# Kernel optimization log

Hardware: AMD Instinct MI355X
Metric: run time of the kernel (lower is better)

## Reference

```python
import jax, jax.numpy as jnp
import numpy as np

N_FACTORS = 4
N_ITERATIONS = 2
N_LAYERS = 2
N_USERS = 50000
N_ITEMS = 50000
EMB_DIM = 128
N_EDGES = 2_000_000
EPS = 1e-12


def setup_inputs() -> dict:
    key = jax.random.key(0)
    k1, k2, k3, k4 = jax.random.split(key, 4)
    n_nodes = N_USERS + N_ITEMS
    return {
        "user_emb": jax.random.normal(k1, (N_USERS, EMB_DIM), dtype=jnp.float32) * 0.1,
        "item_emb": jax.random.normal(k2, (N_ITEMS, EMB_DIM), dtype=jnp.float32) * 0.1,
        "all_h_list": jax.random.randint(k3, (N_EDGES,), 0, n_nodes, dtype=jnp.int32),
        "all_t_list": jax.random.randint(k4, (N_EDGES,), 0, n_nodes, dtype=jnp.int32),
    }


def _l2norm(x):
    # F.normalize(x, dim=1): x / max(||x||_2, eps)
    n = jnp.sqrt(jnp.sum(x * x, axis=1, keepdims=True))
    return x / jnp.maximum(n, EPS)


def _star_routing(user_emb, item_emb, h, t):
    n_nodes = user_emb.shape[0] + item_emb.shape[0]
    E = h.shape[0]
    ego = jnp.concatenate([user_emb, item_emb], axis=0)          # [N, D]
    A_values = jnp.ones((N_FACTORS, E), dtype=ego.dtype)
    all_embeddings = [ego]
    for _layer in range(N_LAYERS):
        ego_chunks = jnp.split(ego, N_FACTORS, axis=1)           # F x [N, D/F]
        layer_chunks = [None] * N_FACTORS
        for it in range(N_ITERATIONS):
            scores = jax.nn.softmax(A_values, axis=0)            # per-edge softmax over factors
            new_vals = []
            for i in range(N_FACTORS):
                v = scores[i]                                    # [E]
                deg = jax.ops.segment_sum(v, h, num_segments=n_nodes)  # row sums of A_i
                d_inv = 1.0 / jnp.sqrt(jnp.maximum(deg, EPS))    # D^{-1/2}
                x = ego_chunks[i] * d_inv[:, None]               # D_col @ e
                # A_i @ x : gather tails, weight by edge value, scatter-add to heads
                x = jax.ops.segment_sum(v[:, None] * x[t], h, num_segments=n_nodes)
                x = x * d_inv[:, None]                           # D_col @ (A @ (D_col @ e))
                layer_chunks[i] = x
                # routing logit update
                head = _l2norm(x[h])                             # [E, D/F]
                tail = _l2norm(ego_chunks[i][t])
                new_vals.append(jnp.sum(head * jnp.tanh(tail), axis=1))
            A_values = A_values + jnp.stack(new_vals, axis=0)
        ego = jnp.concatenate(layer_chunks, axis=1)
        all_embeddings.append(ego)
    # mean over [ego_0, ego_1, ..., ego_L]
    out = jnp.mean(jnp.stack(all_embeddings, axis=1), axis=1)    # [N, D]
    return out


def reference(user_emb, item_emb, all_h_list, all_t_list):
    all_emb = _star_routing(user_emb, item_emb, all_h_list, all_t_list)
    u_g = all_emb[:N_USERS]
    i_g = all_emb[N_USERS:]
    # with pick=False the '_t' (test) path is identical to the train path
    return u_g, i_g, u_g, i_g
```

## Files before the change

### kernel.cpp

```cpp
#include <hip/hip_runtime.h>
#include <cmath>

#define GS_LOOP(i, n) for (int i = blockIdx.x * blockDim.x + threadIdx.x; i < (n); i += gridDim.x * blockDim.x)

constexpr int NUSERS = 50000;
constexpr int NNODES = 100000;
constexpr int EMBD   = 128;
constexpr int NEDGE  = 2000000;
constexpr int NSCAN  = (NNODES + 1023) / 1024;

__device__ __forceinline__ float bf2f(unsigned short u) {
  union { unsigned int i; float f; } v; v.i = ((unsigned int)u) << 16; return v.f;
}
__device__ __forceinline__ unsigned short f2bf(float x) {
  union { float f; unsigned int i; } v; v.f = x;
  unsigned int r = v.i + 0x7FFFu + ((v.i >> 16) & 1u);
  return (unsigned short)(r >> 16);
}

__global__ __launch_bounds__(256) void init_k(const float4* __restrict__ ue4,
                                              const float4* __restrict__ ie4,
                                              float4* __restrict__ ego0,
                                              ushort4* __restrict__ Pb0,
                                              ushort4* __restrict__ Tnb0) {
  const int j = threadIdx.x & 31;
  const int u = blockIdx.x * 8 + (threadIdx.x >> 5);
  if (u >= NNODES) return;
  const float4 y = (u < NUSERS) ? ue4[(size_t)u * 32 + j]
                                : ie4[(size_t)(u - NUSERS) * 32 + j];
  ego0[(size_t)u * 32 + j] = y;
  Pb0[(size_t)u * 32 + j] = make_ushort4(f2bf(y.x), f2bf(y.y), f2bf(y.z), f2bf(y.w));
  float ss = y.x * y.x + y.y * y.y + y.z * y.z + y.w * y.w;
  ss += __shfl_xor(ss, 1, 64);
  ss += __shfl_xor(ss, 2, 64);
  ss += __shfl_xor(ss, 4, 64);
  const float inv = 1.f / fmaxf(sqrtf(ss), 1e-12f);
  Tnb0[(size_t)u * 32 + j] = make_ushort4(f2bf(tanhf(y.x * inv)), f2bf(tanhf(y.y * inv)),
                                          f2bf(tanhf(y.z * inv)), f2bf(tanhf(y.w * inv)));
}

__global__ void hist_k(const int* __restrict__ h, int* __restrict__ counts,
                       float* __restrict__ A) {
  float4* A4 = (float4*)A;
  const float4 ones = make_float4(1.f, 1.f, 1.f, 1.f);
  GS_LOOP(e, NEDGE) { atomicAdd(&counts[h[e]], 1); A4[e] = ones; }
}

__global__ __launch_bounds__(1024) void scan1_k(const int* __restrict__ counts,
                                                int* __restrict__ part,
                                                int* __restrict__ bsum) {
  __shared__ int wsum[16];
  const int tid = threadIdx.x, lane = tid & 63, wid = tid >> 6;
  const int i = blockIdx.x * 1024 + tid;
  int v = (i < NNODES) ? counts[i] : 0;
  #pragma unroll
  for (int off = 1; off < 64; off <<= 1) {
    int y = __shfl_up(v, off, 64);
    if (lane >= off) v += y;
  }
  if (lane == 63) wsum[wid] = v;
  __syncthreads();
  if (wid == 0) {
    int w = (lane < 16) ? wsum[lane] : 0;
    #pragma unroll
    for (int off = 1; off < 16; off <<= 1) {
      int y = __shfl_up(w, off, 64);
      if (lane >= off) w += y;
    }
    if (lane < 16) wsum[lane] = w;
  }
  __syncthreads();
  const int incl = v + (wid ? wsum[wid - 1] : 0);
  if (i < NNODES) part[i] = incl;
  if (tid == 1023) bsum[blockIdx.x] = incl;
}

__global__ __launch_bounds__(128) void scan2_k(const int* __restrict__ bsum,
                                               int* __restrict__ boff) {
  __shared__ int s0[128], s1[128];
  const int tid = threadIdx.x;
  s0[tid] = (tid < NSCAN) ? bsum[tid] : 0;
  __syncthreads();
  int* a = s0; int* b = s1;
  for (int off = 1; off < 128; off <<= 1) {
    const int val = a[tid] + ((tid >= off) ? a[tid - off] : 0);
    b[tid] = val;
    __syncthreads();
    int* tmp = a; a = b; b = tmp;
  }
  boff[tid] = (tid == 0) ? 0 : a[tid - 1];
}

__global__ __launch_bounds__(1024) void scan3_k(const int* __restrict__ part,
                                                const int* __restrict__ boff,
                                                int* __restrict__ row_ptr) {
  const int i = blockIdx.x * 1024 + threadIdx.x;
  if (i < NNODES) row_ptr[i + 1] = part[i] + boff[blockIdx.x];
  if (i == 0) row_ptr[0] = 0;
}

__global__ void fill_k(const int* __restrict__ h, const int* __restrict__ t,
                       const int* __restrict__ row_ptr, int* __restrict__ cur,
                       int* __restrict__ csr_t) {
  GS_LOOP(e, NEDGE) {
    int u = h[e];
    int pos = row_ptr[u] + atomicAdd(&cur[u], 1);
    csr_t[pos] = t[e];
  }
}

__global__ __launch_bounds__(256) void deg_sm_k(const float* __restrict__ A,
                                                const int* __restrict__ row_ptr,
                                                float* __restrict__ c,
                                                float* __restrict__ dv) {
  const float4* A4 = (const float4*)A;
  float4* c4 = (float4*)c;
  const int g = threadIdx.x >> 4;
  const int lane16 = threadIdx.x & 15;
  const int u = blockIdx.x * 16 + g;
  if (u >= NNODES) return;
  const int beg = row_ptr[u], end = row_ptr[u + 1];
  float4 acc = make_float4(0.f, 0.f, 0.f, 0.f);
  for (int p = beg + lane16; p < end; p += 16) {
    float4 a = A4[p];
    float m = fmaxf(fmaxf(a.x, a.y), fmaxf(a.z, a.w));
    float e0 = __expf(a.x - m), e1 = __expf(a.y - m);
    float e2 = __expf(a.z - m), e3 = __expf(a.w - m);
    float inv = 1.f / (e0 + e1 + e2 + e3);
    float4 s = make_float4(e0 * inv, e1 * inv, e2 * inv, e3 * inv);
    c4[p] = s;
    acc.x += s.x; acc.y += s.y; acc.z += s.z; acc.w += s.w;
  }
  #pragma unroll
  for (int m = 1; m < 16; m <<= 1) {
    acc.x += __shfl_xor(acc.x, m, 64);
    acc.y += __shfl_xor(acc.y, m, 64);
    acc.z += __shfl_xor(acc.z, m, 64);
    acc.w += __shfl_xor(acc.w, m, 64);
  }
  if (lane16 == 0)
    ((float4*)dv)[u] = make_float4(rsqrtf(fmaxf(acc.x, 1e-12f)),
                                   rsqrtf(fmaxf(acc.y, 1e-12f)),
                                   rsqrtf(fmaxf(acc.z, 1e-12f)),
                                   rsqrtf(fmaxf(acc.w, 1e-12f)));
}

__global__ __launch_bounds__(256) void prop_k(
    const ushort4* __restrict__ Pb4, float4* __restrict__ Q4,
    const float* __restrict__ dv, const int* __restrict__ row_ptr,
    const int* __restrict__ csr_t, const float* __restrict__ c,
    float* __restrict__ A, const ushort4* __restrict__ Tnb4,
    const float4* __restrict__ e0_4, const float4* __restrict__ e1_4,
    float4* __restrict__ o1_4, ushort4* __restrict__ Pb1w,
    ushort4* __restrict__ Tnb1w, int mode) {
  const int u = blockIdx.x * 4 + (threadIdx.x >> 6);
  const int l = threadIdx.x & 63;
  const int half = l >> 5;
  const int j = l & 31;
  const int f = j >> 3;
  const int beg = row_ptr[u], end = row_ptr[u + 1];

  float4 acc = make_float4(0.f, 0.f, 0.f, 0.f);
  int p = beg + half;
  for (; p + 14 < end; p += 16) {
    const int t0 = csr_t[p],      t1 = csr_t[p + 2];
    const int t2 = csr_t[p + 4],  t3 = csr_t[p + 6];
    const int t4 = csr_t[p + 8],  t5 = csr_t[p + 10];
    const int t6 = csr_t[p + 12], t7 = csr_t[p + 14];
    const ushort4 y0 = Pb4[(size_t)t0 * 32 + j];
    const ushort4 y1 = Pb4[(size_t)t1 * 32 + j];
    const ushort4 y2 = Pb4[(size_t)t2 * 32 + j];
    const ushort4 y3 = Pb4[(size_t)t3 * 32 + j];
    const ushort4 y4 = Pb4[(size_t)t4 * 32 + j];
    const ushort4 y5 = Pb4[(size_t)t5 * 32 + j];
    const ushort4 y6 = Pb4[(size_t)t6 * 32 + j];
    const ushort4 y7 = Pb4[(size_t)t7 * 32 + j];
    const float c0 = c[(size_t)p * 4 + f]        * dv[t0 * 4 + f];
    const float c1 = c[(size_t)(p + 2) * 4 + f]  * dv[t1 * 4 + f];
    const float c2 = c[(size_t)(p + 4) * 4 + f]  * dv[t2 * 4 + f];
    const float c3 = c[(size_t)(p + 6) * 4 + f]  * dv[t3 * 4 + f];
    const float c4_ = c[(size_t)(p + 8) * 4 + f] * dv[t4 * 4 + f];
    const float c5 = c[(size_t)(p + 10) * 4 + f] * dv[t5 * 4 + f];
    const float c6 = c[(size_t)(p + 12) * 4 + f] * dv[t6 * 4 + f];
    const float c7 = c[(size_t)(p + 14) * 4 + f] * dv[t7 * 4 + f];
    acc.x += c0 * bf2f(y0.x) + c1 * bf2f(y1.x) + c2 * bf2f(y2.x) + c3 * bf2f(y3.x)
           + c4_ * bf2f(y4.x) + c5 * bf2f(y5.x) + c6 * bf2f(y6.x) + c7 * bf2f(y7.x);
    acc.y += c0 * bf2f(y0.y) + c1 * bf2f(y1.y) + c2 * bf2f(y2.y) + c3 * bf2f(y3.y)
           + c4_ * bf2f(y4.y) + c5 * bf2f(y5.y) + c6 * bf2f(y6.y) + c7 * bf2f(y7.y);
    acc.z += c0 * bf2f(y0.z) + c1 * bf2f(y1.z) + c2 * bf2f(y2.z) + c3 * bf2f(y3.z)
           + c4_ * bf2f(y4.z) + c5 * bf2f(y5.z) + c6 * bf2f(y6.z) + c7 * bf2f(y7.z);
    acc.w += c0 * bf2f(y0.w) + c1 * bf2f(y1.w) + c2 * bf2f(y2.w) + c3 * bf2f(y3.w)
           + c4_ * bf2f(y4.w) + c5 * bf2f(y5.w) + c6 * bf2f(y6.w) + c7 * bf2f(y7.w);
  }
  for (; p < end; p += 2) {
    const int tn = csr_t[p];
    const float cf = c[(size_t)p * 4 + f] * dv[tn * 4 + f];
    const ushort4 y = Pb4[(size_t)tn * 32 + j];
    acc.x += cf * bf2f(y.x); acc.y += cf * bf2f(y.y);
    acc.z += cf * bf2f(y.z); acc.w += cf * bf2f(y.w);
  }
  acc.x += __shfl_xor(acc.x, 32, 64);
  acc.y += __shfl_xor(acc.y, 32, 64);
  acc.z += __shfl_xor(acc.z, 32, 64);
  acc.w += __shfl_xor(acc.w, 32, 64);
  const float du = dv[u * 4 + f];
  const float4 x = make_float4(acc.x * du, acc.y * du, acc.z * du, acc.w * du);

  if (mode == 2) {
    if (half == 0) {
      const float4 a = e0_4[(size_t)u * 32 + j];
      const float4 b = e1_4[(size_t)u * 32 + j];
      o1_4[(size_t)u * 32 + j] = make_float4((a.x + b.x + x.x) * (1.f / 3.f),
                                             (a.y + b.y + x.y) * (1.f / 3.f),
                                             (a.z + b.z + x.z) * (1.f / 3.f),
                                             (a.w + b.w + x.w) * (1.f / 3.f));
    }
    return;
  }
  if (mode == 1 && half == 0) {
    Q4[(size_t)u * 32 + j] = x;
    Pb1w[(size_t)u * 32 + j] = make_ushort4(f2bf(x.x), f2bf(x.y), f2bf(x.z), f2bf(x.w));
  }

  float ss = x.x * x.x + x.y * x.y + x.z * x.z + x.w * x.w;
  ss += __shfl_xor(ss, 1, 64);
  ss += __shfl_xor(ss, 2, 64);
  ss += __shfl_xor(ss, 4, 64);
  const float inv = 1.f / fmaxf(sqrtf(ss), 1e-12f);
  const float4 xn = make_float4(x.x * inv, x.y * inv, x.z * inv, x.w * inv);
  if (mode == 1 && half == 0)
    Tnb1w[(size_t)u * 32 + j] = make_ushort4(f2bf(tanhf(xn.x)), f2bf(tanhf(xn.y)),
                                             f2bf(tanhf(xn.z)), f2bf(tanhf(xn.w)));

  int q = beg + half;
  for (; q + 6 < end; q += 8) {
    const int t0 = csr_t[q],     t1 = csr_t[q + 2];
    const int t2 = csr_t[q + 4], t3 = csr_t[q + 6];
    const ushort4 b0 = Tnb4[(size_t)t0 * 32 + j];
    const ushort4 b1 = Tnb4[(size_t)t1 * 32 + j];
    const ushort4 b2 = Tnb4[(size_t)t2 * 32 + j];
    const ushort4 b3 = Tnb4[(size_t)t3 * 32 + j];
    float s0 = xn.x * bf2f(b0.x) + xn.y * bf2f(b0.y) + xn.z * bf2f(b0.z) + xn.w * bf2f(b0.w);
    float s1 = xn.x * bf2f(b1.x) + xn.y * bf2f(b1.y) + xn.z * bf2f(b1.z) + xn.w * bf2f(b1.w);
    float s2 = xn.x * bf2f(b2.x) + xn.y * bf2f(b2.y) + xn.z * bf2f(b2.z) + xn.w * bf2f(b2.w);
    float s3 = xn.x * bf2f(b3.x) + xn.y * bf2f(b3.y) + xn.z * bf2f(b3.z) + xn.w * bf2f(b3.w);
    #pragma unroll
    for (int m = 1; m < 8; m <<= 1) {
      s0 += __shfl_xor(s0, m, 64); s1 += __shfl_xor(s1, m, 64);
      s2 += __shfl_xor(s2, m, 64); s3 += __shfl_xor(s3, m, 64);
    }
    if ((j & 7) == 0) {
      A[(size_t)q * 4 + f] += s0;
      A[(size_t)(q + 2) * 4 + f] += s1;
      A[(size_t)(q + 4) * 4 + f] += s2;
      A[(size_t)(q + 6) * 4 + f] += s3;
    }
  }
  for (; q < end; q += 2) {
    const int tn = csr_t[q];
    const ushort4 tb = Tnb4[(size_t)tn * 32 + j];
    float s = xn.x * bf2f(tb.x) + xn.y * bf2f(tb.y) + xn.z * bf2f(tb.z) + xn.w * bf2f(tb.w);
    s += __shfl_xor(s, 1, 64);
    s += __shfl_xor(s, 2, 64);
    s += __shfl_xor(s, 4, 64);
    if ((j & 7) == 0) A[(size_t)q * 4 + f] += s;
  }
}

extern "C" void kernel_launch(void* const* d_in, const int* in_sizes, int n_in,
                              void* d_out, int out_size, void* d_ws, size_t ws_size,
                              hipStream_t stream) {
  const float* ue = (const float*)d_in[0];
  const float* ie = (const float*)d_in[1];
  const int* h = (const int*)d_in[2];
  const int* t = (const int*)d_in[3];
  float* out = (float*)d_out;
  char* ws = (char*)d_ws;

  size_t off = 0;
  auto alloc = [&](size_t bytes) -> void* {
    void* p = ws + off;
    off += (bytes + 255) & ~size_t(255);
    return p;
  };
  float* ego0  = (float*)alloc(sizeof(float) * (size_t)NNODES * EMBD);
  float* ego1  = (float*)alloc(sizeof(float) * (size_t)NNODES * EMBD);
  float* A     = (float*)alloc(sizeof(float) * 4 * (size_t)NEDGE);
  float* c     = (float*)alloc(sizeof(float) * 4 * (size_t)NEDGE);
  float* dv    = (float*)alloc(sizeof(float) * NNODES * 4);
  int* row_ptr = (int*)alloc(sizeof(int) * (NNODES + 1));
  int* cur     = (int*)alloc(sizeof(int) * NNODES);
  int* part    = (int*)alloc(sizeof(int) * NNODES);
  int* bsum    = (int*)alloc(sizeof(int) * 128);
  int* boff    = (int*)alloc(sizeof(int) * 128);
  int* csr_t   = (int*)alloc(sizeof(int) * NEDGE);

  float* o1 = out;
  float* o2 = out + (size_t)NNODES * EMBD;
  ushort4* Pb0  = (ushort4*)o1;
  ushort4* Tnb0 = (ushort4*)((char*)o1 + sizeof(unsigned short) * (size_t)NNODES * EMBD);
  ushort4* Pb1  = (ushort4*)o2;
  ushort4* Tnb1 = (ushort4*)((char*)o2 + sizeof(unsigned short) * (size_t)NNODES * EMBD);

  init_k<<<(NNODES + 7) / 8, 256, 0, stream>>>((const float4*)ue, (const float4*)ie,
                                               (float4*)ego0, Pb0, Tnb0);
  hipMemsetAsync(cur, 0, sizeof(int) * NNODES, stream);
  hist_k<<<2048, 256, 0, stream>>>(h, cur, A);
  scan1_k<<<NSCAN, 1024, 0, stream>>>(cur, part, bsum);
  scan2_k<<<1, 128, 0, stream>>>(bsum, boff);
  scan3_k<<<NSCAN, 1024, 0, stream>>>(part, boff, row_ptr);
  hipMemsetAsync(cur, 0, sizeof(int) * NNODES, stream);
  fill_k<<<2048, 256, 0, stream>>>(h, t, row_ptr, cur, csr_t);

  for (int pass = 0; pass < 4; ++pass) {
    const ushort4* Pb  = (pass < 2) ? Pb0 : Pb1;
    const ushort4* Tnb = (pass < 2) ? Tnb0 : Tnb1;
    const int mode = (pass == 1) ? 1 : (pass == 3) ? 2 : 0;
    deg_sm_k<<<(NNODES + 15) / 16, 256, 0, stream>>>(A, row_ptr, c, dv);
    prop_k<<<NNODES / 4, 256, 0, stream>>>(Pb, (float4*)ego1, dv, row_ptr, csr_t, c, A,
                                           Tnb, (const float4*)ego0, (const float4*)ego1,
                                           (float4*)o1, Pb1, Tnb1, mode);
  }

  hipMemcpyAsync(o2, o1, sizeof(float) * (size_t)NNODES * EMBD,
                 hipMemcpyDeviceToDevice, stream);
}
```

Measured before the change: 1.209 ms.

## Fuse softmax and degree computation into propagation epilogue, specialize first pass

Removes the separate deg_sm_k kernel. The per-edge softmax over factors and the per-node degree sums are now computed in the prop_k epilogue, right after the routing logit update, and written for the next pass into ping-pong dv buffers. The first pass is specialized through template flags to use uniform 0.25 scores and analytic degrees computed in scan3_k, so A no longer needs initializing to ones. Nontemporal loads and stores are added for streaming buffers, and the mode argument becomes a template parameter. This trades four extra kernel launches and one full pass over A and c per iteration for extra shuffles inside the propagation kernel.

```diff
diff --git a/kernel.cpp b/kernel.cpp
--- a/kernel.cpp
+++ b/kernel.cpp
@@ -8,6 +8,9 @@
 constexpr int EMBD   = 128;
 constexpr int NEDGE  = 2000000;
 constexpr int NSCAN  = (NNODES + 1023) / 1024;
+
+typedef float          v4f   __attribute__((ext_vector_type(4)));
+typedef unsigned short v4u16 __attribute__((ext_vector_type(4)));
 
 __device__ __forceinline__ float bf2f(unsigned short u) {
   union { unsigned int i; float f; } v; v.i = ((unsigned int)u) << 16; return v.f;
@@ -39,11 +42,8 @@
                                           f2bf(tanhf(y.z * inv)), f2bf(tanhf(y.w * inv)));
 }
 
-__global__ void hist_k(const int* __restrict__ h, int* __restrict__ counts,
-                       float* __restrict__ A) {
-  float4* A4 = (float4*)A;
-  const float4 ones = make_float4(1.f, 1.f, 1.f, 1.f);
-  GS_LOOP(e, NEDGE) { atomicAdd(&counts[h[e]], 1); A4[e] = ones; }
+__global__ void hist_k(const int* __restrict__ h, int* __restrict__ counts) {
+  GS_LOOP(e, NEDGE) atomicAdd(&counts[h[e]], 1);
 }
 
 __global__ __launch_bounds__(1024) void scan1_k(const int* __restrict__ counts,
@@ -93,9 +93,16 @@
 
 __global__ __launch_bounds__(1024) void scan3_k(const int* __restrict__ part,
                                                 const int* __restrict__ boff,
-                                                int* __restrict__ row_ptr) {
+                                                const int* __restrict__ counts,
+                                                int* __restrict__ row_ptr,
+                                                float* __restrict__ dv0) {
   const int i = blockIdx.x * 1024 + threadIdx.x;
-  if (i < NNODES) row_ptr[i + 1] = part[i] + boff[blockIdx.x];
+  if (i < NNODES) {
+    row_ptr[i + 1] = part[i] + boff[blockIdx.x];
+    const float d = rsqrtf(fmaxf(0.25f * (float)counts[i], 1e-12f));
+    v4f w = {d, d, d, d};
+    *((v4f*)dv0 + i) = w;
+  }
   if (i == 0) row_ptr[0] = 0;
 }
 
@@ -109,50 +116,15 @@
   }
 }
 
-__global__ __launch_bounds__(256) void deg_sm_k(const float* __restrict__ A,
-                                                const int* __restrict__ row_ptr,
-                                                float* __restrict__ c,
-                                                float* __restrict__ dv) {
-  const float4* A4 = (const float4*)A;
-  float4* c4 = (float4*)c;
-  const int g = threadIdx.x >> 4;
-  const int lane16 = threadIdx.x & 15;
-  const int u = blockIdx.x * 16 + g;
-  if (u >= NNODES) return;
-  const int beg = row_ptr[u], end = row_ptr[u + 1];
-  float4 acc = make_float4(0.f, 0.f, 0.f, 0.f);
-  for (int p = beg + lane16; p < end; p += 16) {
-    float4 a = A4[p];
-    float m = fmaxf(fmaxf(a.x, a.y), fmaxf(a.z, a.w));
-    float e0 = __expf(a.x - m), e1 = __expf(a.y - m);
-    float e2 = __expf(a.z - m), e3 = __expf(a.w - m);
-    float inv = 1.f / (e0 + e1 + e2 + e3);
-    float4 s = make_float4(e0 * inv, e1 * inv, e2 * inv, e3 * inv);
-    c4[p] = s;
-    acc.x += s.x; acc.y += s.y; acc.z += s.z; acc.w += s.w;
-  }
-  #pragma unroll
-  for (int m = 1; m < 16; m <<= 1) {
-    acc.x += __shfl_xor(acc.x, m, 64);
-    acc.y += __shfl_xor(acc.y, m, 64);
-    acc.z += __shfl_xor(acc.z, m, 64);
-    acc.w += __shfl_xor(acc.w, m, 64);
-  }
-  if (lane16 == 0)
-    ((float4*)dv)[u] = make_float4(rsqrtf(fmaxf(acc.x, 1e-12f)),
-                                   rsqrtf(fmaxf(acc.y, 1e-12f)),
-                                   rsqrtf(fmaxf(acc.z, 1e-12f)),
-                                   rsqrtf(fmaxf(acc.w, 1e-12f)));
-}
-
+template <int MODE, bool FIRST>
 __global__ __launch_bounds__(256) void prop_k(
     const ushort4* __restrict__ Pb4, float4* __restrict__ Q4,
-    const float* __restrict__ dv, const int* __restrict__ row_ptr,
-    const int* __restrict__ csr_t, const float* __restrict__ c,
-    float* __restrict__ A, const ushort4* __restrict__ Tnb4,
-    const float4* __restrict__ e0_4, const float4* __restrict__ e1_4,
-    float4* __restrict__ o1_4, ushort4* __restrict__ Pb1w,
-    ushort4* __restrict__ Tnb1w, int mode) {
+    const float* __restrict__ dv_in, float* __restrict__ dv_out,
+    const int* __restrict__ row_ptr, const int* __restrict__ csr_t,
+    const float* __restrict__ c, float* __restrict__ A,
+    const ushort4* __restrict__ Tnb4, const float4* __restrict__ e0_4,
+    const float4* __restrict__ e1_4, float4* __restrict__ o1_4,
+    ushort4* __restrict__ Pb1w, ushort4* __restrict__ Tnb1w) {
   const int u = blockIdx.x * 4 + (threadIdx.x >> 6);
   const int l = threadIdx.x & 63;
   const int half = l >> 5;
@@ -175,14 +147,14 @@
     const ushort4 y5 = Pb4[(size_t)t5 * 32 + j];
     const ushort4 y6 = Pb4[(size_t)t6 * 32 + j];
     const ushort4 y7 = Pb4[(size_t)t7 * 32 + j];
-    const float c0 = c[(size_t)p * 4 + f]        * dv[t0 * 4 + f];
-    const float c1 = c[(size_t)(p + 2) * 4 + f]  * dv[t1 * 4 + f];
-    const float c2 = c[(size_t)(p + 4) * 4 + f]  * dv[t2 * 4 + f];
-    const float c3 = c[(size_t)(p + 6) * 4 + f]  * dv[t3 * 4 + f];
-    const float c4_ = c[(size_t)(p + 8) * 4 + f] * dv[t4 * 4 + f];
-    const float c5 = c[(size_t)(p + 10) * 4 + f] * dv[t5 * 4 + f];
-    const float c6 = c[(size_t)(p + 12) * 4 + f] * dv[t6 * 4 + f];
-    const float c7 = c[(size_t)(p + 14) * 4 + f] * dv[t7 * 4 + f];
+    const float c0 = (FIRST ? 0.25f : __builtin_nontemporal_load(c + (size_t)p * 4 + f))        * dv_in[t0 * 4 + f];
+    const float c1 = (FIRST ? 0.25f : __builtin_nontemporal_load(c + (size_t)(p + 2) * 4 + f))  * dv_in[t1 * 4 + f];
+    const float c2 = (FIRST ? 0.25f : __builtin_nontemporal_load(c + (size_t)(p + 4) * 4 + f))  * dv_in[t2 * 4 + f];
+    const float c3 = (FIRST ? 0.25f : __builtin_nontemporal_load(c + (size_t)(p + 6) * 4 + f))  * dv_in[t3 * 4 + f];
+    const float c4_ = (FIRST ? 0.25f : __builtin_nontemporal_load(c + (size_t)(p + 8) * 4 + f)) * dv_in[t4 * 4 + f];
+    const float c5 = (FIRST ? 0.25f : __builtin_nontemporal_load(c + (size_t)(p + 10) * 4 + f)) * dv_in[t5 * 4 + f];
+    const float c6 = (FIRST ? 0.25f : __builtin_nontemporal_load(c + (size_t)(p + 12) * 4 + f)) * dv_in[t6 * 4 + f];
+    const float c7 = (FIRST ? 0.25f : __builtin_nontemporal_load(c + (size_t)(p + 14) * 4 + f)) * dv_in[t7 * 4 + f];
     acc.x += c0 * bf2f(y0.x) + c1 * bf2f(y1.x) + c2 * bf2f(y2.x) + c3 * bf2f(y3.x)
            + c4_ * bf2f(y4.x) + c5 * bf2f(y5.x) + c6 * bf2f(y6.x) + c7 * bf2f(y7.x);
     acc.y += c0 * bf2f(y0.y) + c1 * bf2f(y1.y) + c2 * bf2f(y2.y) + c3 * bf2f(y3.y)
@@ -194,7 +166,7 @@
   }
   for (; p < end; p += 2) {
     const int tn = csr_t[p];
-    const float cf = c[(size_t)p * 4 + f] * dv[tn * 4 + f];
+    const float cf = (FIRST ? 0.25f : __builtin_nontemporal_load(c + (size_t)p * 4 + f)) * dv_in[tn * 4 + f];
     const ushort4 y = Pb4[(size_t)tn * 32 + j];
     acc.x += cf * bf2f(y.x); acc.y += cf * bf2f(y.y);
     acc.z += cf * bf2f(y.z); acc.w += cf * bf2f(y.w);
@@ -203,23 +175,24 @@
   acc.y += __shfl_xor(acc.y, 32, 64);
   acc.z += __shfl_xor(acc.z, 32, 64);
   acc.w += __shfl_xor(acc.w, 32, 64);
-  const float du = dv[u * 4 + f];
+  const float du = dv_in[u * 4 + f];
   const float4 x = make_float4(acc.x * du, acc.y * du, acc.z * du, acc.w * du);
 
-  if (mode == 2) {
+  if (MODE == 2) {
     if (half == 0) {
-      const float4 a = e0_4[(size_t)u * 32 + j];
-      const float4 b = e1_4[(size_t)u * 32 + j];
-      o1_4[(size_t)u * 32 + j] = make_float4((a.x + b.x + x.x) * (1.f / 3.f),
-                                             (a.y + b.y + x.y) * (1.f / 3.f),
-                                             (a.z + b.z + x.z) * (1.f / 3.f),
-                                             (a.w + b.w + x.w) * (1.f / 3.f));
+      const v4f a = __builtin_nontemporal_load((const v4f*)e0_4 + (size_t)u * 32 + j);
+      const v4f b = __builtin_nontemporal_load((const v4f*)e1_4 + (size_t)u * 32 + j);
+      v4f r = {(a.x + b.x + x.x) * (1.f / 3.f), (a.y + b.y + x.y) * (1.f / 3.f),
+               (a.z + b.z + x.z) * (1.f / 3.f), (a.w + b.w + x.w) * (1.f / 3.f)};
+      __builtin_nontemporal_store(r, (v4f*)o1_4 + (size_t)u * 32 + j);
     }
     return;
   }
-  if (mode == 1 && half == 0) {
-    Q4[(size_t)u * 32 + j] = x;
-    Pb1w[(size_t)u * 32 + j] = make_ushort4(f2bf(x.x), f2bf(x.y), f2bf(x.z), f2bf(x.w));
+  if (MODE == 1 && half == 0) {
+    v4f xq = {x.x, x.y, x.z, x.w};
+    __builtin_nontemporal_store(xq, (v4f*)Q4 + (size_t)u * 32 + j);
+    v4u16 pb = {f2bf(x.x), f2bf(x.y), f2bf(x.z), f2bf(x.w)};
+    __builtin_nontemporal_store(pb, (v4u16*)Pb1w + (size_t)u * 32 + j);
   }
 
   float ss = x.x * x.x + x.y * x.y + x.z * x.z + x.w * x.w;
@@ -228,10 +201,27 @@
   ss += __shfl_xor(ss, 4, 64);
   const float inv = 1.f / fmaxf(sqrtf(ss), 1e-12f);
   const float4 xn = make_float4(x.x * inv, x.y * inv, x.z * inv, x.w * inv);
-  if (mode == 1 && half == 0)
-    Tnb1w[(size_t)u * 32 + j] = make_ushort4(f2bf(tanhf(xn.x)), f2bf(tanhf(xn.y)),
-                                             f2bf(tanhf(xn.z)), f2bf(tanhf(xn.w)));
-
+  if (MODE == 1 && half == 0) {
+    v4u16 tb = {f2bf(tanhf(xn.x)), f2bf(tanhf(xn.y)), f2bf(tanhf(xn.z)), f2bf(tanhf(xn.w))};
+    __builtin_nontemporal_store(tb, (v4u16*)Tnb1w + (size_t)u * 32 + j);
+  }
+
+  float dacc = 0.f;
+  auto epi = [&](int ei, float s) {
+    const float aold = FIRST ? 1.f : __builtin_nontemporal_load(A + (size_t)ei * 4 + f);
+    const float anew = aold + s;
+    float mx = fmaxf(anew, __shfl_xor(anew, 8, 64));
+    mx = fmaxf(mx, __shfl_xor(mx, 16, 64));
+    const float ex = __expf(anew - mx);
+    float sm = ex + __shfl_xor(ex, 8, 64);
+    sm += __shfl_xor(sm, 16, 64);
+    const float cv = ex / sm;
+    if ((j & 7) == 0) {
+      __builtin_nontemporal_store(anew, A + (size_t)ei * 4 + f);
+      __builtin_nontemporal_store(cv, (float*)c + (size_t)ei * 4 + f);
+      dacc += cv;
+    }
+  };
   int q = beg + half;
   for (; q + 6 < end; q += 8) {
     const int t0 = csr_t[q],     t1 = csr_t[q + 2];
@@ -249,12 +239,7 @@
       s0 += __shfl_xor(s0, m, 64); s1 += __shfl_xor(s1, m, 64);
       s2 += __shfl_xor(s2, m, 64); s3 += __shfl_xor(s3, m, 64);
     }
-    if ((j & 7) == 0) {
-      A[(size_t)q * 4 + f] += s0;
-      A[(size_t)(q + 2) * 4 + f] += s1;
-      A[(size_t)(q + 4) * 4 + f] += s2;
-      A[(size_t)(q + 6) * 4 + f] += s3;
-    }
+    epi(q, s0); epi(q + 2, s1); epi(q + 4, s2); epi(q + 6, s3);
   }
   for (; q < end; q += 2) {
     const int tn = csr_t[q];
@@ -263,8 +248,11 @@
     s += __shfl_xor(s, 1, 64);
     s += __shfl_xor(s, 2, 64);
     s += __shfl_xor(s, 4, 64);
-    if ((j & 7) == 0) A[(size_t)q * 4 + f] += s;
-  }
+    epi(q, s);
+  }
+  dacc += __shfl_xor(dacc, 32, 64);
+  if (half == 0 && (j & 7) == 0)
+    dv_out[u * 4 + f] = rsqrtf(fmaxf(dacc, 1e-12f));
 }
 
 extern "C" void kernel_launch(void* const* d_in, const int* in_sizes, int n_in,
@@ -287,7 +275,8 @@
   float* ego1  = (float*)alloc(sizeof(float) * (size_t)NNODES * EMBD);
   float* A     = (float*)alloc(sizeof(float) * 4 * (size_t)NEDGE);
   float* c     = (float*)alloc(sizeof(float) * 4 * (size_t)NEDGE);
-  float* dv    = (float*)alloc(sizeof(float) * NNODES * 4);
+  float* dvA   = (float*)alloc(sizeof(float) * NNODES * 4);
+  float* dvB   = (float*)alloc(sizeof(float) * NNODES * 4);
   int* row_ptr = (int*)alloc(sizeof(int) * (NNODES + 1));
   int* cur     = (int*)alloc(sizeof(int) * NNODES);
   int* part    = (int*)alloc(sizeof(int) * NNODES);
@@ -305,22 +294,25 @@
   init_k<<<(NNODES + 7) / 8, 256, 0, stream>>>((const float4*)ue, (const float4*)ie,
                                                (float4*)ego0, Pb0, Tnb0);
   hipMemsetAsync(cur, 0, sizeof(int) * NNODES, stream);
-  hist_k<<<2048, 256, 0, stream>>>(h, cur, A);
+  hist_k<<<2048, 256, 0, stream>>>(h, cur);
   scan1_k<<<NSCAN, 1024, 0, stream>>>(cur, part, bsum);
   scan2_k<<<1, 128, 0, stream>>>(bsum, boff);
-  scan3_k<<<NSCAN, 1024, 0, stream>>>(part, boff, row_ptr);
+  scan3_k<<<NSCAN, 1024, 0, stream>>>(part, boff, cur, row_ptr, dvA);
   hipMemsetAsync(cur, 0, sizeof(int) * NNODES, stream);
   fill_k<<<2048, 256, 0, stream>>>(h, t, row_ptr, cur, csr_t);
 
-  for (int pass = 0; pass < 4; ++pass) {
-    const ushort4* Pb  = (pass < 2) ? Pb0 : Pb1;
-    const ushort4* Tnb = (pass < 2) ? Tnb0 : Tnb1;
-    const int mode = (pass == 1) ? 1 : (pass == 3) ? 2 : 0;
-    deg_sm_k<<<(NNODES + 15) / 16, 256, 0, stream>>>(A, row_ptr, c, dv);
-    prop_k<<<NNODES / 4, 256, 0, stream>>>(Pb, (float4*)ego1, dv, row_ptr, csr_t, c, A,
-                                           Tnb, (const float4*)ego0, (const float4*)ego1,
-                                           (float4*)o1, Pb1, Tnb1, mode);
-  }
+  prop_k<0, true><<<NNODES / 4, 256, 0, stream>>>(
+      Pb0, (float4*)ego1, dvA, dvB, row_ptr, csr_t, c, A, Tnb0,
+      (const float4*)ego0, (const float4*)ego1, (float4*)o1, Pb1, Tnb1);
+  prop_k<1, false><<<NNODES / 4, 256, 0, stream>>>(
+      Pb0, (float4*)ego1, dvB, dvA, row_ptr, csr_t, c, A, Tnb0,
+      (const float4*)ego0, (const float4*)ego1, (float4*)o1, Pb1, Tnb1);
+  prop_k<0, false><<<NNODES / 4, 256, 0, stream>>>(
+      Pb1, (float4*)ego1, dvA, dvB, row_ptr, csr_t, c, A, Tnb1,
+      (const float4*)ego0, (const float4*)ego1, (float4*)o1, Pb1, Tnb1);
+  prop_k<2, false><<<NNODES / 4, 256, 0, stream>>>(
+      Pb1, (float4*)ego1, dvB, dvA, row_ptr, csr_t, c, A, Tnb1,
+      (const float4*)ego0, (const float4*)ego1, (float4*)o1, Pb1, Tnb1);
 
   hipMemcpyAsync(o2, o1, sizeof(float) * (size_t)NNODES * EMBD,
                  hipMemcpyDeviceToDevice, stream);
```

New measurement: 1.327 ms. 1.1x slower.
